# Performance work log

Measured on AMD Instinct MI355X. Metric: run time of the kernel, lower is better.

The kernel has to match this reference:

```python
import jax, jax.numpy as jnp
import numpy as np

B, D, C, H = 65536, 256, 128, 1024
SPLIT = D // 2           # transformed half (odd indices under 'even' mask)
NET_IN = (D - SPLIT) + C # unchanged half + cond


def setup_inputs() -> dict:
    key = jax.random.key(0)
    ks = jax.random.split(key, 10)
    s = 0.02
    return {
        "x": jax.random.normal(ks[0], (B, D), jnp.float32),
        "cond": jax.random.normal(ks[1], (B, C), jnp.float32),
        "W1": jax.random.normal(ks[2], (NET_IN, H), jnp.float32) * s,
        "b1": jnp.zeros((H,), jnp.float32),
        "W2": jax.random.normal(ks[3], (H, H), jnp.float32) * s,
        "b2": jnp.zeros((H,), jnp.float32),
        "Ws": jax.random.normal(ks[4], (H, SPLIT), jnp.float32) * s,
        "bs": jnp.zeros((SPLIT,), jnp.float32),
        "Wt": jax.random.normal(ks[5], (H, SPLIT), jnp.float32) * s,
        "bt": jnp.zeros((SPLIT,), jnp.float32),
    }


def reference(x, cond, W1, b1, W2, b2, Ws, bs, Wt, bt):
    d = x.shape[1]
    even = jnp.arange(0, d, 2)  # mask==1 -> unchanged (x1)
    odd = jnp.arange(1, d, 2)   # mask==0 -> transformed (x2)
    x1u = x[:, even]            # (B, d - d//2)
    x2u = x[:, odd]             # (B, d//2)
    h = jax.nn.relu(jnp.concatenate([x1u, cond], axis=1) @ W1 + b1)
    h = jax.nn.relu(h @ W2 + b2)
    log_s = jnp.tanh(h @ Ws + bs)
    t = h @ Wt + bt
    x2t = x2u * jnp.exp(log_s) + t
    out = jnp.zeros_like(x).at[:, even].set(x1u).at[:, odd].set(x2t)
    log_det = jnp.sum(log_s, axis=1)
    return out, log_det
```

## Files before the change

### kernel.cpp

```cpp
#include <hip/hip_runtime.h>
#include <hip/hip_bf16.h>
#include <math.h>

#define B_ROWS 65536
#define D_DIM 256
#define C_DIM 128
#define H_DIM 1024

typedef __bf16 bf16x8 __attribute__((ext_vector_type(8)));
typedef float f32x4 __attribute__((ext_vector_type(4)));
typedef short short8 __attribute__((ext_vector_type(8)));

__device__ __forceinline__ unsigned short f2bf(float f) {
    unsigned int u = __float_as_uint(f);
    u += 0x7fffu + ((u >> 16) & 1u);
    return (unsigned short)(u >> 16);
}

__device__ __forceinline__ void gl2lds16(const void* g, void* l) {
    __builtin_amdgcn_global_load_lds(
        (const __attribute__((address_space(1))) unsigned int*)g,
        (__attribute__((address_space(3))) unsigned int*)l, 16, 0, 0);
}

__device__ __forceinline__ bf16x8 ds_read_b128_asm(const short* p) {
    bf16x8 r;
    asm volatile("ds_read_b128 %0, %1"
                 : "=v"(r)
                 : "v"((const __attribute__((address_space(3))) short*)p));
    return r;
}

__device__ __forceinline__ int xcd_swz(int id, int nwg) {
    int xcd = id & 7, lid = id >> 3;
    int q = nwg >> 3, r = nwg & 7;
    return (xcd < r ? xcd * (q + 1) : r * (q + 1) + (xcd - r) * q) + lid;
}

__device__ __forceinline__ void swizzle_mn(int id, int mtiles, int& m, int& n) {
    if ((mtiles & 7) == 0) {
        int g = id >> 6, r = id & 63;
        m = g * 8 + (r & 7);
        n = r >> 3;
    } else {
        m = id >> 3;
        n = id & 7;
    }
}

__global__ __launch_bounds__(256) void prep_all(
    const float* __restrict__ W1, const float* __restrict__ W2,
    const float* __restrict__ Ws, const float* __restrict__ Wt,
    const float* __restrict__ bs, const float* __restrict__ bt,
    const float* __restrict__ x, const float* __restrict__ cond,
    short* __restrict__ W1T, short* __restrict__ W2T, short* __restrict__ W3T,
    float* __restrict__ b3, short* __restrict__ A) {
    int t = blockIdx.x * 256 + threadIdx.x;
    if (t < 196864) {
        short8 o;
        if (t < 32768) {
            int n = t >> 5, k0 = (t & 31) << 3;
#pragma unroll
            for (int j = 0; j < 8; ++j) o[j] = (short)f2bf(W1[(size_t)(k0 + j) * 1024 + n]);
            *(short8*)&W1T[(size_t)n * 256 + k0] = o;
        } else if (t < 163840) {
            int u = t - 32768;
            int n = u >> 7, k0 = (u & 127) << 3;
#pragma unroll
            for (int j = 0; j < 8; ++j) o[j] = (short)f2bf(W2[(size_t)(k0 + j) * 1024 + n]);
            *(short8*)&W2T[(size_t)n * 1024 + k0] = o;
        } else if (t < 180224) {
            int u = t - 163840;
            int n = u >> 7, k0 = (u & 127) << 3;
#pragma unroll
            for (int j = 0; j < 8; ++j) o[j] = (short)f2bf(Ws[(size_t)(k0 + j) * 128 + n]);
            *(short8*)&W3T[(size_t)n * 1024 + k0] = o;
        } else if (t < 196608) {
            int u = t - 180224;
            int n = u >> 7, k0 = (u & 127) << 3;
#pragma unroll
            for (int j = 0; j < 8; ++j) o[j] = (short)f2bf(Wt[(size_t)(k0 + j) * 128 + n]);
            *(short8*)&W3T[131072 + (size_t)n * 1024 + k0] = o;
        } else {
            int i = t - 196608;
            b3[i] = (i < 128) ? bs[i] : bt[i - 128];
        }
    } else {
        int u = t - 196864;
        int m = u >> 5, seg = u & 31;
        short8 o;
        if (seg < 16) {
            const float4* p = (const float4*)(x + (size_t)m * 256 + seg * 16);
            float4 a = p[0], b = p[1], c = p[2], d = p[3];
            o[0] = (short)f2bf(a.x); o[1] = (short)f2bf(a.z);
            o[2] = (short)f2bf(b.x); o[3] = (short)f2bf(b.z);
            o[4] = (short)f2bf(c.x); o[5] = (short)f2bf(c.z);
            o[6] = (short)f2bf(d.x); o[7] = (short)f2bf(d.z);
        } else {
            const float4* p = (const float4*)(cond + (size_t)m * 128 + (seg - 16) * 8);
            float4 a = p[0], b = p[1];
            o[0] = (short)f2bf(a.x); o[1] = (short)f2bf(a.y);
            o[2] = (short)f2bf(a.z); o[3] = (short)f2bf(a.w);
            o[4] = (short)f2bf(b.x); o[5] = (short)f2bf(b.y);
            o[6] = (short)f2bf(b.z); o[7] = (short)f2bf(b.w);
        }
        *(short8*)&A[(size_t)m * 256 + seg * 8] = o;
    }
}

__global__ __launch_bounds__(256) void gemm_tn(
    const short* __restrict__ A, const short* __restrict__ Bw,
    const float* __restrict__ bias, unsigned short* __restrict__ Cout,
    int mtiles, int N, int K) {
    constexpr int BK = 64;
    __shared__ __align__(16) short As[128 * BK];
    __shared__ __align__(16) short Bs[128 * BK];
    const int tid = threadIdx.x;
    const int lane = tid & 63;
    const int wave = tid >> 6;
    int mt, nt;
    swizzle_mn(blockIdx.x, mtiles, mt, nt);
    const int tm = mt * 128, tn = nt * 128;
    const int mo = (wave >> 1) * 64;
    const int no = (wave & 1) * 64;

    f32x4 acc[4][4];
#pragma unroll
    for (int i = 0; i < 4; ++i)
#pragma unroll
        for (int j = 0; j < 4; ++j) acc[i][j] = f32x4{0.f, 0.f, 0.f, 0.f};

    const int srow = lane >> 3;
    const int skb = (lane & 7) ^ srow;

    for (int kc = 0; kc < K; kc += BK) {
        __syncthreads();
#pragma unroll
        for (int i = 0; i < 4; ++i) {
            int c = wave * 4 + i;
            int row = c * 8 + srow;
            gl2lds16(A + (size_t)(tm + row) * K + kc + skb * 8, &As[c * 512]);
            gl2lds16(Bw + (size_t)(tn + row) * K + kc + skb * 8, &Bs[c * 512]);
        }
        __syncthreads();
#pragma unroll
        for (int kk = 0; kk < 2; ++kk) {
            bf16x8 af[4], bfr[4];
            int kb = kk * 4 + (lane >> 4);
#pragma unroll
            for (int t = 0; t < 4; ++t) {
                int r = mo + t * 16 + (lane & 15);
                af[t] = *(const bf16x8*)&As[r * BK + ((kb ^ (r & 7)) << 3)];
                int n = no + t * 16 + (lane & 15);
                bfr[t] = *(const bf16x8*)&Bs[n * BK + ((kb ^ (n & 7)) << 3)];
            }
#pragma unroll
            for (int i = 0; i < 4; ++i)
#pragma unroll
                for (int j = 0; j < 4; ++j)
                    acc[i][j] = __builtin_amdgcn_mfma_f32_16x16x32_bf16(
                        af[i], bfr[j], acc[i][j], 0, 0, 0);
        }
    }

#pragma unroll
    for (int j = 0; j < 4; ++j) {
        int col = tn + no + j * 16 + (lane & 15);
        float bb = bias[col];
#pragma unroll
        for (int i = 0; i < 4; ++i) {
            int row0 = tm + mo + i * 16 + ((lane >> 4) << 2);
            f32x4 v = acc[i][j];
#pragma unroll
            for (int rr = 0; rr < 4; ++rr)
                Cout[(size_t)(row0 + rr) * N + col] = f2bf(fmaxf(v[rr] + bb, 0.f));
        }
    }
}

template<int K>
__global__ __launch_bounds__(512, 2) void gemm2_8ph(
    const short* __restrict__ A, const short* __restrict__ Bw,
    const float* __restrict__ bias, unsigned short* __restrict__ Cout) {
    constexpr int NT = K / 64;
    constexpr unsigned OFF_A0 = 0, OFF_B0 = 16384, OFF_A1 = 32768, OFF_B1 = 49152;
    __shared__ __align__(16) short smem[65536];

    const int tid = threadIdx.x;
    const int lane = tid & 63;
    const int wave = tid >> 6;
    const int wm = wave >> 2;
    const int wn = wave & 3;
    const int l15 = lane & 15;
    const int quad = lane >> 4;
    const int srow = lane >> 3;
    const int skb8 = ((lane & 7) ^ srow) << 3;

    const int wgid = xcd_swz(blockIdx.x, gridDim.x);
    const int mt = wgid >> 2, nt = wgid & 3;
    const size_t Abase = (size_t)(mt * 256) * K;
    const size_t Bbase = (size_t)(nt * 256) * K;

    f32x4 acc[8][4];
#pragma unroll
    for (int m = 0; m < 8; ++m)
#pragma unroll
        for (int n = 0; n < 4; ++n) acc[m][n] = f32x4{0.f, 0.f, 0.f, 0.f};

    bf16x8 af[2][2] = {};
    bf16x8 bfr[4][2] = {};

    auto stage2 = [&](unsigned off, const short* g, size_t rowbase, int kc, int c0, int c1) {
        gl2lds16(g + rowbase + (size_t)(c0 * 8 + srow) * K + kc + skb8, smem + off + c0 * 512);
        gl2lds16(g + rowbase + (size_t)(c1 * 8 + srow) * K + kc + skb8, smem + off + c1 * 512);
    };
    auto stageU = [&](int u, unsigned aOff, unsigned bOff, int kc) {
        if (u == 0)      stage2(bOff, Bw, Bbase, kc, wave * 2, wave * 2 + 1);
        else if (u == 1) stage2(bOff, Bw, Bbase, kc, 16 + wave * 2, 17 + wave * 2);
        else if (u == 2) stage2(aOff, A, Abase, kc, wave, 16 + wave);
        else             stage2(aOff, A, Abase, kc, 8 + wave, 24 + wave);
    };

    const unsigned x0 = (unsigned)((quad ^ (l15 & 7)) << 3);
    const unsigned x1 = (unsigned)(((4 + quad) ^ (l15 & 7)) << 3);

    auto mfma8 = [&](int pprev) {
        __builtin_amdgcn_s_setprio(1);
#pragma unroll
        for (int kk = 0; kk < 2; ++kk)
#pragma unroll
            for (int mm = 0; mm < 2; ++mm)
#pragma unroll
                for (int n = 0; n < 4; ++n)
                    acc[pprev * 2 + mm][n] = __builtin_amdgcn_mfma_f32_16x16x32_bf16(
                        af[mm][kk], bfr[n][kk], acc[pprev * 2 + mm][n], 0, 0, 0);
        __builtin_amdgcn_s_setprio(0);
    };

    auto slot = [&](int ph, int w, unsigned caOff, unsigned cbOff,
                    unsigned naOff, unsigned nbOff) {
        if (ph & 1) {
            if (w < NT - 2) asm volatile("s_waitcnt vmcnt(6)" ::: "memory");
            else            asm volatile("s_waitcnt vmcnt(0)" ::: "memory");
        }
        __builtin_amdgcn_sched_barrier(0);
        __builtin_amdgcn_s_barrier();
        __builtin_amdgcn_sched_barrier(0);
        if (ph == 0) { if (w + 1 < NT) stageU(3, naOff, nbOff, (w + 1) << 6); }
        else         { if (w + 2 < NT) stageU(ph - 1, caOff, cbOff, (w + 2) << 6); }
        __builtin_amdgcn_sched_barrier(0);
        asm volatile("s_waitcnt lgkmcnt(0)" ::: "memory");
        __builtin_amdgcn_sched_barrier(0);
        mfma8((ph + 3) & 3);
        __builtin_amdgcn_sched_barrier(0);
        const short* aA = smem + caOff + ((wm << 7) + l15) * 64;
        const short* aB = smem + cbOff + ((wn << 6) + l15) * 64;
        if (ph == 0) {
#pragma unroll
            for (int n = 0; n < 4; ++n) {
                bfr[n][0] = ds_read_b128_asm(aB + n * 1024 + x0);
                bfr[n][1] = ds_read_b128_asm(aB + n * 1024 + x1);
            }
        }
#pragma unroll
        for (int mm = 0; mm < 2; ++mm) {
            af[mm][0] = ds_read_b128_asm(aA + (ph * 2 + mm) * 1024 + x0);
            af[mm][1] = ds_read_b128_asm(aA + (ph * 2 + mm) * 1024 + x1);
        }
        __builtin_amdgcn_sched_barrier(0);
    };

    stageU(0, OFF_A0, OFF_B0, 0);
    stageU(1, OFF_A0, OFF_B0, 0);
    stageU(2, OFF_A0, OFF_B0, 0);
    stageU(3, OFF_A0, OFF_B0, 0);
    stageU(0, OFF_A1, OFF_B1, 64);
    stageU(1, OFF_A1, OFF_B1, 64);
    stageU(2, OFF_A1, OFF_B1, 64);
    asm volatile("s_waitcnt vmcnt(6)" ::: "memory");

#pragma unroll 1
    for (int w = 0; w < NT; w += 2) {
#pragma unroll
        for (int ph = 0; ph < 4; ++ph)
            slot(ph, w, OFF_A0, OFF_B0, OFF_A1, OFF_B1);
#pragma unroll
        for (int ph = 0; ph < 4; ++ph)
            slot(ph, w + 1, OFF_A1, OFF_B1, OFF_A0, OFF_B0);
    }
    asm volatile("s_waitcnt lgkmcnt(0)" ::: "memory");
    __builtin_amdgcn_sched_barrier(0);
    mfma8(3);

    __syncthreads();
    unsigned short* cs = (unsigned short*)smem;
#pragma unroll
    for (int n = 0; n < 4; ++n) {
        int colblk = wn * 4 + n;
        int col = (colblk << 4) + l15;
        float bb = bias[nt * 256 + col];
#pragma unroll
        for (int m = 0; m < 8; ++m) {
            int row = (wm << 7) + m * 16 + (quad << 2);
#pragma unroll
            for (int rr = 0; rr < 4; ++rr) {
                int rw = row + rr;
                int sb = colblk ^ ((rw >> 2) & 3);
                cs[rw * 256 + (sb << 4) + l15] = f2bf(fmaxf(acc[m][n][rr] + bb, 0.f));
            }
        }
    }
    __syncthreads();
    const size_t cbase = (size_t)(mt * 256) * 1024 + nt * 256;
    const int rloc = tid >> 5, cchunk = tid & 31;
#pragma unroll
    for (int rnd = 0; rnd < 16; ++rnd) {
        int rw = rnd * 16 + rloc;
        int blk = cchunk >> 1, half = cchunk & 1;
        int sb = blk ^ ((rw >> 2) & 3);
        short8 v = *(const short8*)&cs[rw * 256 + (sb << 4) + half * 8];
        *(short8*)((unsigned short*)Cout + cbase + (size_t)rw * 1024 + cchunk * 8) = v;
    }
}

__global__ __launch_bounds__(512, 2) void gemm3_pipe(
    const short* __restrict__ H2, const short* __restrict__ W3T,
    const float* __restrict__ b3, const float* __restrict__ x,
    float* __restrict__ out, float* __restrict__ logdet) {
    constexpr int K = 1024, NT = 16;
    constexpr unsigned OFF_A0 = 0, OFF_B0 = 8192, OFF_A1 = 24576, OFF_B1 = 32768;
    __shared__ __align__(16) short smem[49152];
    __shared__ float rowsum[128];

    const int tid = threadIdx.x;
    const int lane = tid & 63;
    const int wave = tid >> 6;
    const int wm = wave >> 2;
    const int wn = wave & 3;
    const int l15 = lane & 15;
    const int quad = lane >> 4;
    const int srow = lane >> 3;
    const int skb8 = ((lane & 7) ^ srow) << 3;

    const int mt = xcd_swz(blockIdx.x, gridDim.x);
    const int tm = mt * 128;
    const size_t Abase = (size_t)tm * K;

    if (tid < 128) rowsum[tid] = 0.f;

    f32x4 acc[4][4];
#pragma unroll
    for (int i = 0; i < 4; ++i)
#pragma unroll
        for (int j = 0; j < 4; ++j) acc[i][j] = f32x4{0.f, 0.f, 0.f, 0.f};

    bf16x8 af[2] = {};
    bf16x8 bfr[4][2] = {};

    auto stage2 = [&](unsigned off, const short* g, size_t rowbase, int kc, int c0, int c1) {
        gl2lds16(g + rowbase + (size_t)(c0 * 8 + srow) * K + kc + skb8, smem + off + c0 * 512);
        gl2lds16(g + rowbase + (size_t)(c1 * 8 + srow) * K + kc + skb8, smem + off + c1 * 512);
    };
    auto stageA  = [&](unsigned aOff, int kc) { stage2(aOff, H2, Abase, kc, wave, 8 + wave); };
    auto stageB1 = [&](unsigned bOff, int kc) { stage2(bOff, W3T, 0, kc, 2 * wave, 2 * wave + 1); };
    auto stageB2 = [&](unsigned bOff, int kc) { stage2(bOff, W3T, 0, kc, 16 + 2 * wave, 17 + 2 * wave); };

    const unsigned x0 = (unsigned)((quad ^ (l15 & 7)) << 3);
    const unsigned x1 = (unsigned)(((4 + quad) ^ (l15 & 7)) << 3);

    auto mfma4 = [&](int pprev) {
        __builtin_amdgcn_s_setprio(1);
#pragma unroll
        for (int kk = 0; kk < 2; ++kk)
#pragma unroll
            for (int n = 0; n < 4; ++n)
                acc[pprev][n] = __builtin_amdgcn_mfma_f32_16x16x32_bf16(
                    af[kk], bfr[n][kk], acc[pprev][n], 0, 0, 0);
        __builtin_amdgcn_s_setprio(0);
    };

    auto slot = [&](int ph, int w, unsigned caOff, unsigned cbOff, unsigned naOff) {
        if (w < NT - 2) asm volatile("s_waitcnt vmcnt(4)" ::: "memory");
        else            asm volatile("s_waitcnt vmcnt(0)" ::: "memory");
        __builtin_amdgcn_sched_barrier(0);
        __builtin_amdgcn_s_barrier();
        __builtin_amdgcn_sched_barrier(0);
        if (ph == 0)      { if (w + 1 < NT) stageA(naOff, (w + 1) << 6); }
        else if (ph == 1) { if (w + 2 < NT) stageB1(cbOff, (w + 2) << 6); }
        else if (ph == 2) { if (w + 2 < NT) stageB2(cbOff, (w + 2) << 6); }
        __builtin_amdgcn_sched_barrier(0);
        asm volatile("s_waitcnt lgkmcnt(0)" ::: "memory");
        __builtin_amdgcn_sched_barrier(0);
        mfma4((ph + 3) & 3);
        __builtin_amdgcn_sched_barrier(0);
        const short* aA = smem + caOff + ((wm << 6) + l15) * 64;
        const short* aB = smem + cbOff + ((wn << 6) + l15) * 64;
        if (ph == 0) {
#pragma unroll
            for (int n = 0; n < 4; ++n) {
                bfr[n][0] = ds_read_b128_asm(aB + n * 1024 + x0);
                bfr[n][1] = ds_read_b128_asm(aB + n * 1024 + x1);
            }
        }
        af[0] = ds_read_b128_asm(aA + ph * 1024 + x0);
        af[1] = ds_read_b128_asm(aA + ph * 1024 + x1);
        __builtin_amdgcn_sched_barrier(0);
    };

    stageA(OFF_A0, 0);
    stageB1(OFF_B0, 0);
    stageB2(OFF_B0, 0);
    stageB1(OFF_B1, 64);
    stageB2(OFF_B1, 64);
    asm volatile("s_waitcnt vmcnt(4)" ::: "memory");

#pragma unroll 1
    for (int w = 0; w < NT; w += 2) {
#pragma unroll
        for (int ph = 0; ph < 4; ++ph)
            slot(ph, w, OFF_A0, OFF_B0, OFF_A1);
#pragma unroll
        for (int ph = 0; ph < 4; ++ph)
            slot(ph, w + 1, OFF_A1, OFF_B1, OFF_A0);
    }
    asm volatile("s_waitcnt lgkmcnt(0)" ::: "memory");
    __builtin_amdgcn_sched_barrier(0);
    mfma4(3);

    __syncthreads();
    float* Tbuf = (float*)smem;
    if (wn >= 2) {
#pragma unroll
        for (int n = 0; n < 4; ++n) {
            int col = (wn << 6) + n * 16 + l15;
            float bb = b3[col];
            int cl = col - 128;
#pragma unroll
            for (int mm = 0; mm < 4; ++mm) {
#pragma unroll
                for (int rr = 0; rr < 4; ++rr) {
                    int m = (wm << 6) + mm * 16 + quad * 4 + rr;
                    Tbuf[m * 132 + cl] = acc[mm][n][rr] + bb;
                }
            }
        }
    }
    __syncthreads();
    if (wn < 2) {
#pragma unroll
        for (int mm = 0; mm < 4; ++mm) {
#pragma unroll
            for (int rr = 0; rr < 4; ++rr) {
                int m = (wm << 6) + mm * 16 + quad * 4 + rr;
                int grow = tm + m;
                float s = 0.f;
#pragma unroll
                for (int n = 0; n < 4; ++n) {
                    int j = (wn << 6) + n * 16 + l15;
                    float p = acc[mm][n][rr] + b3[j];
                    p = fminf(fmaxf(p, -15.f), 15.f);
                    float e2 = __expf(2.f * p);
                    float ls = (e2 - 1.f) / (e2 + 1.f);
                    s += ls;
                    float tt = Tbuf[m * 132 + j];
                    float2 xv = *(const float2*)&x[(size_t)grow * 256 + 2 * j];
                    float2 ov;
                    ov.x = xv.x;
                    ov.y = xv.y * __expf(ls) + tt;
                    *(float2*)&out[(size_t)grow * 256 + 2 * j] = ov;
                }
                s += __shfl_xor(s, 1);
                s += __shfl_xor(s, 2);
                s += __shfl_xor(s, 4);
                s += __shfl_xor(s, 8);
                if (l15 == 0) atomicAdd(&rowsum[m], s);
            }
        }
    }
    __syncthreads();
    if (tid < 128) logdet[tm + tid] = rowsum[tid];
}

extern "C" void kernel_launch(void* const* d_in, const int* in_sizes, int n_in,
                              void* d_out, int out_size, void* d_ws, size_t ws_size,
                              hipStream_t stream) {
    const float* x = (const float*)d_in[0];
    const float* cond = (const float*)d_in[1];
    const float* W1 = (const float*)d_in[2];
    const float* b1 = (const float*)d_in[3];
    const float* W2 = (const float*)d_in[4];
    const float* b2 = (const float*)d_in[5];
    const float* Wsp = (const float*)d_in[6];
    const float* bs = (const float*)d_in[7];
    const float* Wtp = (const float*)d_in[8];
    const float* bt = (const float*)d_in[9];

    char* ws = (char*)d_ws;
    short* W1T = (short*)(ws);
    short* W2T = (short*)(ws + 524288ull);
    short* W3T = (short*)(ws + 2621440ull);
    float* b3  = (float*)(ws + 3145728ull);
    short* Aprep = (short*)(ws + 3149824ull);
    const size_t chunk_base = 3149824ull + 33554432ull;

    int n_chunks = 1;
    while (n_chunks < 512) {
        size_t rp = (size_t)B_ROWS / n_chunks;
        if (chunk_base + rp * 4096ull <= ws_size) break;
        n_chunks *= 2;
    }
    const size_t RP = (size_t)B_ROWS / n_chunks;

    float* out = (float*)d_out;
    float* logdet = out + (size_t)B_ROWS * D_DIM;

    prep_all<<<(196864 + B_ROWS * 32 + 255) / 256, 256, 0, stream>>>(
        W1, W2, Wsp, Wtp, bs, bt, x, cond, W1T, W2T, W3T, b3, Aprep);

    for (int c = 0; c < n_chunks; ++c) {
        const size_t r0 = (size_t)c * RP;
        short* H1 = (short*)(ws + chunk_base);
        short* H2 = (short*)(ws + chunk_base + 2048ull * RP);
        const int mtiles = (int)(RP / 128);

        if ((RP & 255) == 0) {
            gemm2_8ph<256><<<(int)(RP / 256) * 4, 512, 0, stream>>>(
                Aprep + r0 * 256, W1T, b1, (unsigned short*)H1);
            gemm2_8ph<1024><<<(int)(RP / 256) * 4, 512, 0, stream>>>(
                H1, W2T, b2, (unsigned short*)H2);
        } else {
            gemm_tn<<<mtiles * 8, 256, 0, stream>>>(
                Aprep + r0 * 256, W1T, b1, (unsigned short*)H1, mtiles, H_DIM, 256);
            gemm_tn<<<mtiles * 8, 256, 0, stream>>>(
                H1, W2T, b2, (unsigned short*)H2, mtiles, H_DIM, H_DIM);
        }
        gemm3_pipe<<<(int)(RP / 128), 512, 0, stream>>>(
            H2, W3T, b3, x + r0 * D_DIM, out + r0 * D_DIM, logdet + r0);
    }
}
```

Measured before the change: 427.3 us.

## Double-buffer MFMA operand registers to overlap LDS reads with matrix math

Adds a second register set for the A and B fragments so each slot issues the LDS reads for the next phase before running the MFMAs on the previous phase's fragments. The full lgkmcnt(0) drain is replaced by a partial wait that lets the new ds_reads stay in flight while the MFMAs execute. This is meant to hide LDS read latency behind tensor-core work. The cost is higher VGPR pressure, which may reduce occupancy or cause spills, and the hand-tuned lgkmcnt values must match the number of reads issued.

```diff
diff --git a/kernel.cpp b/kernel.cpp
--- a/kernel.cpp
+++ b/kernel.cpp
@@ -207,8 +207,8 @@
 #pragma unroll
         for (int n = 0; n < 4; ++n) acc[m][n] = f32x4{0.f, 0.f, 0.f, 0.f};
 
-    bf16x8 af[2][2] = {};
-    bf16x8 bfr[4][2] = {};
+    bf16x8 af[2][2][2] = {};
+    bf16x8 bfr[2][4][2] = {};
 
     auto stage2 = [&](unsigned off, const short* g, size_t rowbase, int kc, int c0, int c1) {
         gl2lds16(g + rowbase + (size_t)(c0 * 8 + srow) * K + kc + skb8, smem + off + c0 * 512);
@@ -224,7 +224,7 @@
     const unsigned x0 = (unsigned)((quad ^ (l15 & 7)) << 3);
     const unsigned x1 = (unsigned)(((4 + quad) ^ (l15 & 7)) << 3);
 
-    auto mfma8 = [&](int pprev) {
+    auto mfma8 = [&](int pprev, int aset, int wset) {
         __builtin_amdgcn_s_setprio(1);
 #pragma unroll
         for (int kk = 0; kk < 2; ++kk)
@@ -233,11 +233,11 @@
 #pragma unroll
                 for (int n = 0; n < 4; ++n)
                     acc[pprev * 2 + mm][n] = __builtin_amdgcn_mfma_f32_16x16x32_bf16(
-                        af[mm][kk], bfr[n][kk], acc[pprev * 2 + mm][n], 0, 0, 0);
+                        af[aset][mm][kk], bfr[wset][n][kk], acc[pprev * 2 + mm][n], 0, 0, 0);
         __builtin_amdgcn_s_setprio(0);
     };
 
-    auto slot = [&](int ph, int w, unsigned caOff, unsigned cbOff,
+    auto slot = [&](int ph, int w, int wpar, unsigned caOff, unsigned cbOff,
                     unsigned naOff, unsigned nbOff) {
         if (ph & 1) {
             if (w < NT - 2) asm volatile("s_waitcnt vmcnt(6)" ::: "memory");
@@ -249,24 +249,26 @@
         if (ph == 0) { if (w + 1 < NT) stageU(3, naOff, nbOff, (w + 1) << 6); }
         else         { if (w + 2 < NT) stageU(ph - 1, caOff, cbOff, (w + 2) << 6); }
         __builtin_amdgcn_sched_barrier(0);
-        asm volatile("s_waitcnt lgkmcnt(0)" ::: "memory");
-        __builtin_amdgcn_sched_barrier(0);
-        mfma8((ph + 3) & 3);
-        __builtin_amdgcn_sched_barrier(0);
         const short* aA = smem + caOff + ((wm << 7) + l15) * 64;
         const short* aB = smem + cbOff + ((wn << 6) + l15) * 64;
+        const int sp = ph & 1;
         if (ph == 0) {
 #pragma unroll
             for (int n = 0; n < 4; ++n) {
-                bfr[n][0] = ds_read_b128_asm(aB + n * 1024 + x0);
-                bfr[n][1] = ds_read_b128_asm(aB + n * 1024 + x1);
+                bfr[wpar][n][0] = ds_read_b128_asm(aB + n * 1024 + x0);
+                bfr[wpar][n][1] = ds_read_b128_asm(aB + n * 1024 + x1);
             }
         }
 #pragma unroll
         for (int mm = 0; mm < 2; ++mm) {
-            af[mm][0] = ds_read_b128_asm(aA + (ph * 2 + mm) * 1024 + x0);
-            af[mm][1] = ds_read_b128_asm(aA + (ph * 2 + mm) * 1024 + x1);
-        }
+            af[sp][mm][0] = ds_read_b128_asm(aA + (ph * 2 + mm) * 1024 + x0);
+            af[sp][mm][1] = ds_read_b128_asm(aA + (ph * 2 + mm) * 1024 + x1);
+        }
+        __builtin_amdgcn_sched_barrier(0);
+        if (ph == 0) asm volatile("s_waitcnt lgkmcnt(12)" ::: "memory");
+        else         asm volatile("s_waitcnt lgkmcnt(4)" ::: "memory");
+        __builtin_amdgcn_sched_barrier(0);
+        mfma8((ph + 3) & 3, sp ^ 1, (ph == 0) ? (wpar ^ 1) : wpar);
         __builtin_amdgcn_sched_barrier(0);
     };
 
@@ -283,14 +285,14 @@
     for (int w = 0; w < NT; w += 2) {
 #pragma unroll
         for (int ph = 0; ph < 4; ++ph)
-            slot(ph, w, OFF_A0, OFF_B0, OFF_A1, OFF_B1);
+            slot(ph, w, 0, OFF_A0, OFF_B0, OFF_A1, OFF_B1);
 #pragma unroll
         for (int ph = 0; ph < 4; ++ph)
-            slot(ph, w + 1, OFF_A1, OFF_B1, OFF_A0, OFF_B0);
+            slot(ph, w + 1, 1, OFF_A1, OFF_B1, OFF_A0, OFF_B0);
     }
     asm volatile("s_waitcnt lgkmcnt(0)" ::: "memory");
     __builtin_amdgcn_sched_barrier(0);
-    mfma8(3);
+    mfma8(3, 1, 1);
 
     __syncthreads();
     unsigned short* cs = (unsigned short*)smem;
```

New measurement: 577.0 us. +35.0%, slower.
